# Kernel optimization log

Measured on AMD Instinct MI355X. Metric: run time of the kernel, lower is better.

Reference implementation:

```python
import jax, jax.numpy as jnp
import numpy as np

Q_HEADS = 16
KV_HEADS = 4
ROPE_THETA = 10000.0


def _rope(x, seq_len):
    # x: [B, S, H, D]; pairs are consecutive along D (view_as_complex semantics)
    D = x.shape[-1]
    inv_freq = 1.0 / (ROPE_THETA ** (jnp.arange(0, D, 2, dtype=jnp.float32) / D))
    freqs = jnp.arange(seq_len, dtype=jnp.float32)[:, None] * inv_freq  # [S, D/2]
    cos = jnp.cos(freqs)[None, :, None, :]
    sin = jnp.sin(freqs)[None, :, None, :]
    xr = x.reshape(x.shape[:-1] + (D // 2, 2))
    x0, x1 = xr[..., 0], xr[..., 1]
    out = jnp.stack([x0 * cos - x1 * sin, x0 * sin + x1 * cos], axis=-1)
    return out.reshape(x.shape)


def setup_inputs() -> dict:
    key = jax.random.key(0)
    ks = jax.random.split(key, 6)
    B, S, E = 1, 2048, 2048
    KV_DIM = KV_HEADS * (E // Q_HEADS)  # 512
    scale = 0.02
    return {
        "x": jax.random.normal(ks[0], (B, S, E), dtype=jnp.float32),
        "Wq": jax.random.normal(ks[1], (E, E), dtype=jnp.float32) * scale,
        "Wk": jax.random.normal(ks[2], (KV_DIM, E), dtype=jnp.float32) * scale,
        "Wv": jax.random.normal(ks[3], (KV_DIM, E), dtype=jnp.float32) * scale,
        "Wo": jax.random.normal(ks[4], (E, E), dtype=jnp.float32) * scale,
        "bo": jax.random.normal(ks[5], (E,), dtype=jnp.float32) * scale,
        "cache_keys": jnp.zeros((B, S, KV_HEADS, E // Q_HEADS), dtype=jnp.float32),
        "cache_value": jnp.zeros((B, S, KV_HEADS, E // Q_HEADS), dtype=jnp.float32),
        "start_pos": 0,
    }


def reference(x, Wq, Wk, Wv, Wo, bo, cache_keys, cache_value, start_pos):
    B, S, E = x.shape
    hd = E // Q_HEADS
    G = Q_HEADS // KV_HEADS  # queries per kv head

    xq = (x @ Wq.T).reshape(B, S, Q_HEADS, hd)
    xk = (x @ Wk.T).reshape(B, S, KV_HEADS, hd)
    xv = (x @ Wv.T).reshape(B, S, KV_HEADS, hd)

    # Original applies RoPE with positions 0..seq_len-1 for both q and k
    # (freq tensor is sliced [:seq_len] inside apply_rotry_position_embedding).
    xq = _rope(xq, S)
    xk = _rope(xk, S)

    # cache write at start_pos (static python int)
    cache_keys = jax.lax.dynamic_update_slice(cache_keys, xk, (0, start_pos, 0, 0))
    cache_value = jax.lax.dynamic_update_slice(cache_value, xv, (0, start_pos, 0, 0))
    total = start_pos + S
    k_full = cache_keys[:, :total]   # [B, T, KVH, hd]
    v_full = cache_value[:, :total]

    # repeat_interleave over the head axis == GQA expansion
    k = jnp.repeat(k_full, G, axis=2)  # [B, T, QH, hd]
    v = jnp.repeat(v_full, G, axis=2)

    scores = jnp.einsum("bshd,bthd->bhst", xq, k) / jnp.sqrt(jnp.float32(hd))
    causal = jnp.triu(jnp.ones((S, total), dtype=bool), k=1)  # [S, T]
    scores = jnp.where(causal[None, None, :, :], -jnp.inf, scores)
    weights = jax.nn.softmax(scores, axis=-1)
    out = jnp.einsum("bhst,bthd->bshd", weights, v).reshape(B, S, E)
    # dropout p=0.0 / eval mode -> identity
    return out @ Wo.T + bo
```

## Files before the change

### kernel.cpp

```cpp
#include <hip/hip_runtime.h>
#include <stdint.h>

typedef unsigned short u16;
typedef float  f32x4  __attribute__((ext_vector_type(4)));
typedef __bf16 bf16x8 __attribute__((ext_vector_type(8)));
typedef __bf16 bf16x4 __attribute__((ext_vector_type(4)));
typedef unsigned short u16x8 __attribute__((ext_vector_type(8)));
typedef unsigned short u16x4v __attribute__((ext_vector_type(4)));

#define S_LEN 2048
#define E_DIM 2048
#define HD    128
#define QH    16
#define KVH   4
#define KVD   512
#define NQKV  3072
#define QK_SCALE 0.08838834764831845f

#define AS1 __attribute__((address_space(1)))
#define AS3 __attribute__((address_space(3)))

__device__ __forceinline__ u16 f2bf(float f) {
  union { float f; uint32_t u; } v; v.f = f;
  return (u16)((v.u + 0x7FFFu + ((v.u >> 16) & 1u)) >> 16);
}

__global__ void cast_all_kernel(const float* __restrict__ x, const float* __restrict__ Wq,
                                const float* __restrict__ Wk, const float* __restrict__ Wv,
                                const float* __restrict__ Wo,
                                u16* __restrict__ xb, u16* __restrict__ Wcat,
                                u16* __restrict__ Wob, float2* __restrict__ tab) {
  int i = blockIdx.x * blockDim.x + threadIdx.x;
  if (i >= 3670016) {
    int j = i - 3670016;
    int s = j >> 6, pidx = j & 63;
    float inv = exp2f((float)pidx * (-13.287712379549449f / 64.0f));
    float sn, cs;
    sincosf((float)s * inv, &sn, &cs);
    tab[j] = make_float2(cs, sn);
    return;
  }
  const float* src; u16* dst;
  if (i < (1 << 20))                       { src = x  + (size_t)i * 4;  dst = xb + (size_t)i * 4; }
  else if (i < (2 << 20))                  { size_t j = i - (1 << 20);  src = Wq + j * 4; dst = Wcat + j * 4; }
  else if (i < (2 << 20) + (1 << 18))      { size_t j = i - (2 << 20);  src = Wk + j * 4; dst = Wcat + (size_t)E_DIM * E_DIM + j * 4; }
  else if (i < (2 << 20) + (2 << 18))      { size_t j = i - (2 << 20) - (1 << 18); src = Wv + j * 4; dst = Wcat + (size_t)(E_DIM + KVD) * E_DIM + j * 4; }
  else                                     { size_t j = i - (2 << 20) - (2 << 18); src = Wo + j * 4; dst = Wob + j * 4; }
  float4 f = *reinterpret_cast<const float4*>(src);
  u16x4v o;
  o[0] = f2bf(f.x); o[1] = f2bf(f.y); o[2] = f2bf(f.z); o[3] = f2bf(f.w);
  *reinterpret_cast<u16x4v*>(dst) = o;
}

template<bool BIAS, int MODE>
__global__ __launch_bounds__(256) void gemm_bt_kernel(
    const u16* __restrict__ A, const u16* __restrict__ B,
    float* __restrict__ C, const float* __restrict__ bias,
    const float2* __restrict__ tab, u16* __restrict__ qb,
    u16* __restrict__ kb, u16* __restrict__ vTp,
    int M, int N, int K)
{
  __shared__ u16 As[2][64 * 64];
  __shared__ u16 Bs[2][128 * 64];

  const int tid  = threadIdx.x;
  const int lane = tid & 63;
  const int wid  = tid >> 6;
  const int wc   = wid * 32;
  const int lr   = lane & 15;
  const int kg   = lane >> 4;
  const int sw   = lr & 7;

  const int bm = blockIdx.y * 64;
  const int bn = blockIdx.x * 128;

  f32x4 acc[4][2];
  #pragma unroll
  for (int r = 0; r < 4; ++r)
    #pragma unroll
    for (int c = 0; c < 2; ++c) acc[r][c] = (f32x4){0.f, 0.f, 0.f, 0.f};

  const int srow   = wid * 8 + (lane >> 3);
  const int schunk = (lane & 7) ^ (lane >> 3);

  const u16* gA = A + (size_t)(bm + srow) * K + schunk * 8;
  const u16* gB = B + (size_t)(bn + srow) * K + schunk * 8;

  auto stage = [&](int buf, int kt) {
    #pragma unroll
    for (int i = 0; i < 2; ++i)
      __builtin_amdgcn_global_load_lds(
          (const AS1 void*)(gA + (size_t)i * 32 * K + kt),
          (AS3 void*)(&As[buf][(wid*8 + i*32) * 64]), 16, 0, 0);
    #pragma unroll
    for (int i = 0; i < 4; ++i)
      __builtin_amdgcn_global_load_lds(
          (const AS1 void*)(gB + (size_t)i * 32 * K + kt),
          (AS3 void*)(&Bs[buf][(wid*8 + i*32) * 64]), 16, 0, 0);
  };

  stage(0, 0);
  __syncthreads();

  int cur = 0;
  for (int kt = 0; kt < K; kt += 64) {
    if (kt + 64 < K) stage(cur ^ 1, kt + 64);
    #pragma unroll
    for (int kk = 0; kk < 2; ++kk) {
      bf16x8 af[4], bfr[2];
      #pragma unroll
      for (int r = 0; r < 4; ++r)
        af[r] = *reinterpret_cast<const bf16x8*>(
            &As[cur][(r*16 + lr)*64 + ((kk*4 + kg) ^ sw)*8]);
      #pragma unroll
      for (int c = 0; c < 2; ++c)
        bfr[c] = *reinterpret_cast<const bf16x8*>(
            &Bs[cur][(wc + c*16 + lr)*64 + ((kk*4 + kg) ^ sw)*8]);
      #pragma unroll
      for (int r = 0; r < 4; ++r)
        #pragma unroll
        for (int c = 0; c < 2; ++c)
          acc[r][c] = __builtin_amdgcn_mfma_f32_16x16x32_bf16(af[r], bfr[c], acc[r][c], 0, 0, 0);
    }
    __syncthreads();
    cur ^= 1;
  }

  const int crow = kg * 4;
  #pragma unroll
  for (int r = 0; r < 4; ++r) {
    #pragma unroll
    for (int c = 0; c < 2; ++c) {
      int gr = bm + r*16 + crow;
      int gc = bn + wc + c*16 + lr;
      if constexpr (MODE == 0) {
        float badd = BIAS ? bias[gc] : 0.0f;
        #pragma unroll
        for (int reg = 0; reg < 4; ++reg)
          C[(size_t)(gr + reg)*N + gc] = acc[r][c][reg] + badd;
      } else {
        if (gc < E_DIM + KVD) {
          int pidx = (gc & 127) >> 1;
          bool odd = lr & 1;
          #pragma unroll
          for (int reg = 0; reg < 4; ++reg) {
            float val = acc[r][c][reg];
            float oth = __shfl_xor(val, 1);
            float2 cs = tab[(gr + reg) * 64 + pidx];
            float o = odd ? (oth * cs.y + val * cs.x)
                          : (val * cs.x - oth * cs.y);
            if (gc < E_DIM)
              qb[(size_t)(gr + reg) * E_DIM + gc] = f2bf(o * QK_SCALE);
            else
              kb[(size_t)(gr + reg) * KVD + (gc - E_DIM)] = f2bf(o);
          }
        } else {
          bf16x4 pk;
          #pragma unroll
          for (int reg = 0; reg < 4; ++reg) pk[reg] = (__bf16)acc[r][c][reg];
          *reinterpret_cast<bf16x4*>(
              &vTp[(size_t)(gc - E_DIM - KVD) * S_LEN + gr]) = pk;
        }
      }
    }
  }
}

__device__ __forceinline__ void attn_tile(
    int t, int qt, int wid, int lr, int kg,
    const bf16x8* qf, f32x4* o, float& mr, float& ls,
    const u16* ks, const u16* vts, u16* ps)
{
  const int sw = lr & 7;
  f32x4 st[4];
  #pragma unroll
  for (int c = 0; c < 4; ++c) st[c] = (f32x4){0.f, 0.f, 0.f, 0.f};
  __builtin_amdgcn_s_setprio(1);
  #pragma unroll
  for (int kk = 0; kk < 4; ++kk) {
    #pragma unroll
    for (int c = 0; c < 4; ++c) {
      bf16x8 kfr = *reinterpret_cast<const bf16x8*>(
          &ks[(c*16 + lr)*128 + ((kk*4 + kg) ^ sw)*8]);
      st[c] = __builtin_amdgcn_mfma_f32_16x16x32_bf16(kfr, qf[kk], st[c], 0, 0, 0);
    }
  }
  __builtin_amdgcn_s_setprio(0);
  if (t == qt) {
    #pragma unroll
    for (int c = 0; c < 4; ++c)
      #pragma unroll
      for (int reg = 0; reg < 4; ++reg)
        if (c*16 + kg*4 + reg > wid*16 + lr) st[c][reg] = -1e30f;
  }
  float cm[4];
  #pragma unroll
  for (int c = 0; c < 4; ++c)
    cm[c] = fmaxf(fmaxf(st[c][0], st[c][1]), fmaxf(st[c][2], st[c][3]));
  float pm = fmaxf(fmaxf(cm[0], cm[1]), fmaxf(cm[2], cm[3]));
  pm = fmaxf(pm, __shfl_xor(pm, 16));
  pm = fmaxf(pm, __shfl_xor(pm, 32));

  if (!__all(pm - mr <= 8.0f)) {
    float nm = fmaxf(mr, pm);
    float alpha = __expf(mr - nm);
    ls *= alpha;
    mr = nm;
    float ar[4];
    #pragma unroll
    for (int reg = 0; reg < 4; ++reg)
      ar[reg] = __shfl(alpha, kg*4 + reg);
    #pragma unroll
    for (int d = 0; d < 8; ++d)
      #pragma unroll
      for (int reg = 0; reg < 4; ++reg)
        o[d][reg] *= ar[reg];
  }

  float p[4][4];
  float csum[4];
  #pragma unroll
  for (int c = 0; c < 4; ++c) {
    #pragma unroll
    for (int reg = 0; reg < 4; ++reg)
      p[c][reg] = __expf(st[c][reg] - mr);
    csum[c] = (p[c][0] + p[c][1]) + (p[c][2] + p[c][3]);
  }
  float sum = (csum[0] + csum[1]) + (csum[2] + csum[3]);
  sum += __shfl_xor(sum, 16);
  sum += __shfl_xor(sum, 32);
  ls += sum;

  #pragma unroll
  for (int c = 0; c < 4; ++c) {
    bf16x4 pk;
    #pragma unroll
    for (int reg = 0; reg < 4; ++reg) pk[reg] = (__bf16)p[c][reg];
    *reinterpret_cast<bf16x4*>(&ps[lr*72 + c*16 + kg*4]) = pk;
  }
  __builtin_amdgcn_s_setprio(1);
  #pragma unroll
  for (int kk = 0; kk < 2; ++kk) {
    bf16x8 pa = *reinterpret_cast<const bf16x8*>(&ps[lr*72 + kk*32 + kg*8]);
    #pragma unroll
    for (int d = 0; d < 8; ++d) {
      bf16x8 vb = *reinterpret_cast<const bf16x8*>(
          &vts[(d*16 + lr)*64 + ((kk*4 + kg) ^ sw)*8]);
      o[d] = __builtin_amdgcn_mfma_f32_16x16x32_bf16(pa, vb, o[d], 0, 0, 0);
    }
  }
  __builtin_amdgcn_s_setprio(0);
}

__global__ __launch_bounds__(256, 2) void attn_kernel(
    const u16* __restrict__ Q, const u16* __restrict__ Kc,
    const u16* __restrict__ VT, u16* __restrict__ Out)
{
  __shared__ u16 Ks[2][64 * 128];
  __shared__ u16 VTs[2][128 * 64];
  __shared__ u16 Ps[4][16 * 72];

  const int x = blockIdx.x;
  int qt, h;
  if (x < 256) { qt = x & 31; h = x >> 5; }
  else         { int xp = x - 256; qt = 31 - (xp & 31); h = 8 + (xp >> 5); }
  const int kvh = h >> 2;
  const int tid  = threadIdx.x;
  const int lane = tid & 63;
  const int wid  = tid >> 6;
  const int lr   = lane & 15;
  const int kg   = lane >> 4;

  const int NT = qt + 1;

  bf16x8 qf[4];
  {
    const u16* qa = Q + (size_t)(qt*64 + wid*16 + lr) * E_DIM + h * HD + kg * 8;
    #pragma unroll
    for (int kk = 0; kk < 4; ++kk)
      qf[kk] = *reinterpret_cast<const bf16x8*>(qa + kk * 32);
  }

  f32x4 o[8];
  #pragma unroll
  for (int d = 0; d < 8; ++d) o[d] = (f32x4){0.f,0.f,0.f,0.f};
  float mr = -1e30f, ls = 0.f;

  u16x8 kreg[4], vreg[4];
  const u16* kbase = Kc + kvh * HD;
  const u16* vbase = VT + (size_t)(kvh * HD) * S_LEN;

  auto stage_load = [&](int t) {
    #pragma unroll
    for (int i = 0; i < 4; ++i) {
      int c = i * 256 + tid;
      kreg[i] = *reinterpret_cast<const u16x8*>(
          kbase + (size_t)(t*64 + (c >> 4)) * KVD + (c & 15) * 8);
      vreg[i] = *reinterpret_cast<const u16x8*>(
          vbase + (size_t)(c >> 3) * S_LEN + t*64 + (c & 7) * 8);
    }
  };
  auto stage_write = [&](int b) {
    #pragma unroll
    for (int i = 0; i < 4; ++i) {
      int c = i * 256 + tid;
      int kr = c >> 4, kc = c & 15;
      *reinterpret_cast<u16x8*>(&Ks[b][kr*128 + (kc ^ (kr & 7))*8]) = kreg[i];
      int vr = c >> 3, vc = c & 7;
      *reinterpret_cast<u16x8*>(&VTs[b][vr*64 + (vc ^ (vr & 7))*8]) = vreg[i];
    }
  };

  int p = 0;
  stage_load(0);
  stage_write(0);
  __syncthreads();

  for (int t = 0; t < NT; ++t) {
    if (t + 1 < NT) stage_load(t + 1);
    attn_tile(t, qt, wid, lr, kg, qf, o, mr, ls, Ks[p], VTs[p], Ps[wid]);
    if (t + 1 < NT) {
      stage_write(p ^ 1);
      __syncthreads();
      p ^= 1;
    }
  }

  {
    float inv = 1.0f / ls;
    float ivq[4];
    #pragma unroll
    for (int reg = 0; reg < 4; ++reg)
      ivq[reg] = __shfl(inv, kg*4 + reg);
    #pragma unroll
    for (int reg = 0; reg < 4; ++reg) {
      int grow = qt*64 + wid*16 + kg*4 + reg;
      #pragma unroll
      for (int d = 0; d < 8; ++d)
        Out[(size_t)grow * E_DIM + h * HD + d*16 + lr] =
            __builtin_bit_cast(u16, (__bf16)(o[d][reg] * ivq[reg]));
    }
  }
}

extern "C" void kernel_launch(void* const* d_in, const int* in_sizes, int n_in,
                              void* d_out, int out_size, void* d_ws, size_t ws_size,
                              hipStream_t stream)
{
  const float* x  = (const float*)d_in[0];
  const float* Wq = (const float*)d_in[1];
  const float* Wk = (const float*)d_in[2];
  const float* Wv = (const float*)d_in[3];
  const float* Wo = (const float*)d_in[4];
  const float* bo = (const float*)d_in[5];
  float* out = (float*)d_out;

  char* w = (char*)d_ws;
  u16*    xb   = (u16*)(w);
  u16*    Wcat = (u16*)(w + (8u  << 20));
  u16*    Wob  = (u16*)(w + (20u << 20));
  float2* tab  = (float2*)(w + (28u << 20));
  u16*    qb   = (u16*)(w + (30u << 20));
  u16*    kb   = (u16*)(w + (38u << 20));
  u16*    vT   = (u16*)(w + (40u << 20));
  u16*    attn = (u16*)(w + (42u << 20));
  (void)ws_size; (void)in_sizes; (void)n_in; (void)out_size;

  cast_all_kernel<<<14848, 256, 0, stream>>>(x, Wq, Wk, Wv, Wo, xb, Wcat, Wob, tab);

  gemm_bt_kernel<false, 2><<<dim3(NQKV/128, S_LEN/64), 256, 0, stream>>>(
      xb, Wcat, nullptr, nullptr, tab, qb, kb, vT, S_LEN, NQKV, E_DIM);

  attn_kernel<<<512, 256, 0, stream>>>(qb, kb, vT, attn);

  gemm_bt_kernel<true, 0><<<dim3(E_DIM/128, S_LEN/64), 256, 0, stream>>>(
      attn, Wob, out, bo, nullptr, nullptr, nullptr, nullptr, S_LEN, E_DIM, E_DIM);
}
```

Before: 133.8 us.

## Switch attention to 32x32x16 MFMA with split-KV waves and final merge

Rewrites the attention inner loop to use 32x32x16 bf16 MFMA instead of 16x16x32. The four waves now form a 2x2 grid: two 32-row query groups times two 32-column halves of each KV tile. Each wave keeps its own online-softmax state, and the halves are merged through shared memory at the end. The P tile is rearranged into the A-operand layout with cross-lane shuffles rather than an LDS round trip, which removes the Ps buffer. This is meant to cut LDS traffic and MFMA instruction count per tile, at the cost of more accumulator registers, an extra epilogue sync and merge, and per-wave softmax state.

```diff
diff --git a/kernel.cpp b/kernel.cpp
--- a/kernel.cpp
+++ b/kernel.cpp
@@ -3,10 +3,13 @@
 
 typedef unsigned short u16;
 typedef float  f32x4  __attribute__((ext_vector_type(4)));
+typedef float  f32x16 __attribute__((ext_vector_type(16)));
 typedef __bf16 bf16x8 __attribute__((ext_vector_type(8)));
 typedef __bf16 bf16x4 __attribute__((ext_vector_type(4)));
 typedef unsigned short u16x8 __attribute__((ext_vector_type(8)));
 typedef unsigned short u16x4v __attribute__((ext_vector_type(4)));
+typedef unsigned int u32x2 __attribute__((ext_vector_type(2)));
+typedef unsigned int u32x4 __attribute__((ext_vector_type(4)));
 
 #define S_LEN 2048
 #define E_DIM 2048
@@ -166,99 +169,12 @@
   }
 }
 
-__device__ __forceinline__ void attn_tile(
-    int t, int qt, int wid, int lr, int kg,
-    const bf16x8* qf, f32x4* o, float& mr, float& ls,
-    const u16* ks, const u16* vts, u16* ps)
-{
-  const int sw = lr & 7;
-  f32x4 st[4];
-  #pragma unroll
-  for (int c = 0; c < 4; ++c) st[c] = (f32x4){0.f, 0.f, 0.f, 0.f};
-  __builtin_amdgcn_s_setprio(1);
-  #pragma unroll
-  for (int kk = 0; kk < 4; ++kk) {
-    #pragma unroll
-    for (int c = 0; c < 4; ++c) {
-      bf16x8 kfr = *reinterpret_cast<const bf16x8*>(
-          &ks[(c*16 + lr)*128 + ((kk*4 + kg) ^ sw)*8]);
-      st[c] = __builtin_amdgcn_mfma_f32_16x16x32_bf16(kfr, qf[kk], st[c], 0, 0, 0);
-    }
-  }
-  __builtin_amdgcn_s_setprio(0);
-  if (t == qt) {
-    #pragma unroll
-    for (int c = 0; c < 4; ++c)
-      #pragma unroll
-      for (int reg = 0; reg < 4; ++reg)
-        if (c*16 + kg*4 + reg > wid*16 + lr) st[c][reg] = -1e30f;
-  }
-  float cm[4];
-  #pragma unroll
-  for (int c = 0; c < 4; ++c)
-    cm[c] = fmaxf(fmaxf(st[c][0], st[c][1]), fmaxf(st[c][2], st[c][3]));
-  float pm = fmaxf(fmaxf(cm[0], cm[1]), fmaxf(cm[2], cm[3]));
-  pm = fmaxf(pm, __shfl_xor(pm, 16));
-  pm = fmaxf(pm, __shfl_xor(pm, 32));
-
-  if (!__all(pm - mr <= 8.0f)) {
-    float nm = fmaxf(mr, pm);
-    float alpha = __expf(mr - nm);
-    ls *= alpha;
-    mr = nm;
-    float ar[4];
-    #pragma unroll
-    for (int reg = 0; reg < 4; ++reg)
-      ar[reg] = __shfl(alpha, kg*4 + reg);
-    #pragma unroll
-    for (int d = 0; d < 8; ++d)
-      #pragma unroll
-      for (int reg = 0; reg < 4; ++reg)
-        o[d][reg] *= ar[reg];
-  }
-
-  float p[4][4];
-  float csum[4];
-  #pragma unroll
-  for (int c = 0; c < 4; ++c) {
-    #pragma unroll
-    for (int reg = 0; reg < 4; ++reg)
-      p[c][reg] = __expf(st[c][reg] - mr);
-    csum[c] = (p[c][0] + p[c][1]) + (p[c][2] + p[c][3]);
-  }
-  float sum = (csum[0] + csum[1]) + (csum[2] + csum[3]);
-  sum += __shfl_xor(sum, 16);
-  sum += __shfl_xor(sum, 32);
-  ls += sum;
-
-  #pragma unroll
-  for (int c = 0; c < 4; ++c) {
-    bf16x4 pk;
-    #pragma unroll
-    for (int reg = 0; reg < 4; ++reg) pk[reg] = (__bf16)p[c][reg];
-    *reinterpret_cast<bf16x4*>(&ps[lr*72 + c*16 + kg*4]) = pk;
-  }
-  __builtin_amdgcn_s_setprio(1);
-  #pragma unroll
-  for (int kk = 0; kk < 2; ++kk) {
-    bf16x8 pa = *reinterpret_cast<const bf16x8*>(&ps[lr*72 + kk*32 + kg*8]);
-    #pragma unroll
-    for (int d = 0; d < 8; ++d) {
-      bf16x8 vb = *reinterpret_cast<const bf16x8*>(
-          &vts[(d*16 + lr)*64 + ((kk*4 + kg) ^ sw)*8]);
-      o[d] = __builtin_amdgcn_mfma_f32_16x16x32_bf16(pa, vb, o[d], 0, 0, 0);
-    }
-  }
-  __builtin_amdgcn_s_setprio(0);
-}
-
 __global__ __launch_bounds__(256, 2) void attn_kernel(
     const u16* __restrict__ Q, const u16* __restrict__ Kc,
     const u16* __restrict__ VT, u16* __restrict__ Out)
 {
   __shared__ u16 Ks[2][64 * 128];
   __shared__ u16 VTs[2][128 * 64];
-  __shared__ u16 Ps[4][16 * 72];
 
   const int x = blockIdx.x;
   int qt, h;
@@ -268,22 +184,26 @@
   const int tid  = threadIdx.x;
   const int lane = tid & 63;
   const int wid  = tid >> 6;
-  const int lr   = lane & 15;
-  const int kg   = lane >> 4;
+  const int kvg  = wid & 1;
+  const int rowg = wid >> 1;
+  const int ln   = lane & 31;
+  const int hi   = lane >> 5;
 
   const int NT = qt + 1;
 
-  bf16x8 qf[4];
+  bf16x8 qf[8];
   {
-    const u16* qa = Q + (size_t)(qt*64 + wid*16 + lr) * E_DIM + h * HD + kg * 8;
-    #pragma unroll
-    for (int kk = 0; kk < 4; ++kk)
-      qf[kk] = *reinterpret_cast<const bf16x8*>(qa + kk * 32);
-  }
-
-  f32x4 o[8];
+    const u16* qa = Q + (size_t)(qt*64 + rowg*32 + ln) * E_DIM + h * HD + hi * 8;
+    #pragma unroll
+    for (int ks = 0; ks < 8; ++ks)
+      qf[ks] = *reinterpret_cast<const bf16x8*>(qa + ks * 16);
+  }
+
+  f32x16 o4[4];
   #pragma unroll
-  for (int d = 0; d < 8; ++d) o[d] = (f32x4){0.f,0.f,0.f,0.f};
+  for (int d = 0; d < 4; ++d)
+    #pragma unroll
+    for (int r = 0; r < 16; ++r) o4[d][r] = 0.f;
   float mr = -1e30f, ls = 0.f;
 
   u16x8 kreg[4], vreg[4];
@@ -316,9 +236,96 @@
   stage_write(0);
   __syncthreads();
 
+  const int krow = kvg*32 + ln;
+
   for (int t = 0; t < NT; ++t) {
     if (t + 1 < NT) stage_load(t + 1);
-    attn_tile(t, qt, wid, lr, kg, qf, o, mr, ls, Ks[p], VTs[p], Ps[wid]);
+
+    f32x16 st;
+    #pragma unroll
+    for (int r = 0; r < 16; ++r) st[r] = 0.f;
+    __builtin_amdgcn_s_setprio(1);
+    #pragma unroll
+    for (int ks = 0; ks < 8; ++ks) {
+      bf16x8 kfr = *reinterpret_cast<const bf16x8*>(
+          &Ks[p][krow*128 + ((ks*2 + hi) ^ (ln & 7))*8]);
+      st = __builtin_amdgcn_mfma_f32_32x32x16_bf16(kfr, qf[ks], st, 0, 0, 0);
+    }
+    __builtin_amdgcn_s_setprio(0);
+
+    if (t == qt) {
+      #pragma unroll
+      for (int reg = 0; reg < 16; ++reg) {
+        int kvl = kvg*32 + 4*hi + (reg & 3) + 8*(reg >> 2);
+        if (kvl > rowg*32 + ln) st[reg] = -1e30f;
+      }
+    }
+
+    float pm = -1e30f;
+    #pragma unroll
+    for (int reg = 0; reg < 16; ++reg) pm = fmaxf(pm, st[reg]);
+    pm = fmaxf(pm, __shfl_xor(pm, 32));
+
+    if (!__all(pm - mr <= 8.0f)) {
+      float nm = fmaxf(mr, pm);
+      float alpha = __expf(mr - nm);
+      ls *= alpha;
+      mr = nm;
+      #pragma unroll
+      for (int reg = 0; reg < 16; ++reg) {
+        int crow = (reg & 3) + 8*(reg >> 2) + 4*hi;
+        float ar = __shfl(alpha, crow);
+        #pragma unroll
+        for (int d = 0; d < 4; ++d) o4[d][reg] *= ar;
+      }
+    }
+
+    float pv[16];
+    float sum = 0.f;
+    #pragma unroll
+    for (int reg = 0; reg < 16; ++reg) {
+      pv[reg] = __expf(st[reg] - mr);
+      sum += pv[reg];
+    }
+    sum += __shfl_xor(sum, 32);
+    ls += sum;
+
+    bf16x8 pa[2];
+    #pragma unroll
+    for (int ks = 0; ks < 2; ++ks) {
+      bf16x4 A4, B4;
+      #pragma unroll
+      for (int j = 0; j < 4; ++j) {
+        A4[j] = (__bf16)pv[ks*8 + j];
+        B4[j] = (__bf16)pv[ks*8 + 4 + j];
+      }
+      u32x2 uA = __builtin_bit_cast(u32x2, A4);
+      u32x2 uB = __builtin_bit_cast(u32x2, B4);
+      unsigned sx = hi ? uA[0] : uB[0];
+      unsigned sy = hi ? uA[1] : uB[1];
+      unsigned rx = __shfl_xor(sx, 32);
+      unsigned ry = __shfl_xor(sy, 32);
+      u32x4 w;
+      w[0] = hi ? rx : uA[0];
+      w[1] = hi ? ry : uA[1];
+      w[2] = hi ? uB[0] : rx;
+      w[3] = hi ? uB[1] : ry;
+      pa[ks] = __builtin_bit_cast(bf16x8, w);
+    }
+
+    __builtin_amdgcn_s_setprio(1);
+    #pragma unroll
+    for (int d = 0; d < 4; ++d) {
+      int vrow = d*32 + ln;
+      #pragma unroll
+      for (int ks = 0; ks < 2; ++ks) {
+        bf16x8 vb = *reinterpret_cast<const bf16x8*>(
+            &VTs[p][vrow*64 + ((kvg*4 + ks*2 + hi) ^ (ln & 7))*8]);
+        o4[d] = __builtin_amdgcn_mfma_f32_32x32x16_bf16(pa[ks], vb, o4[d], 0, 0, 0);
+      }
+    }
+    __builtin_amdgcn_s_setprio(0);
+
     if (t + 1 < NT) {
       stage_write(p ^ 1);
       __syncthreads();
@@ -326,19 +333,41 @@
     }
   }
 
-  {
-    float inv = 1.0f / ls;
-    float ivq[4];
-    #pragma unroll
-    for (int reg = 0; reg < 4; ++reg)
-      ivq[reg] = __shfl(inv, kg*4 + reg);
-    #pragma unroll
-    for (int reg = 0; reg < 4; ++reg) {
-      int grow = qt*64 + wid*16 + kg*4 + reg;
-      #pragma unroll
-      for (int d = 0; d < 8; ++d)
-        Out[(size_t)grow * E_DIM + h * HD + d*16 + lr] =
-            __builtin_bit_cast(u16, (__bf16)(o[d][reg] * ivq[reg]));
+  __syncthreads();
+  float* Obuf = (float*)&Ks[0][0];
+  float* Lbuf = (float*)&VTs[0][0];
+  if (kvg == 1) {
+    if (hi == 0) { Lbuf[rowg*32 + ln] = mr; Lbuf[64 + rowg*32 + ln] = ls; }
+    #pragma unroll
+    for (int reg = 0; reg < 16; ++reg) {
+      int crow = (reg & 3) + 8*(reg >> 2) + 4*hi;
+      #pragma unroll
+      for (int d = 0; d < 4; ++d)
+        Obuf[(rowg*32 + crow)*128 + d*32 + ln] = o4[d][reg];
+    }
+  }
+  __syncthreads();
+  if (kvg == 0) {
+    float mB = Lbuf[rowg*32 + ln];
+    float lB = Lbuf[64 + rowg*32 + ln];
+    float m  = fmaxf(mr, mB);
+    float a0 = __expf(mr - m);
+    float a1 = __expf(mB - m);
+    float inv = 1.0f / (ls*a0 + lB*a1);
+    #pragma unroll
+    for (int reg = 0; reg < 16; ++reg) {
+      int crow = (reg & 3) + 8*(reg >> 2) + 4*hi;
+      float a0r = __shfl(a0, crow);
+      float a1r = __shfl(a1, crow);
+      float ivr = __shfl(inv, crow);
+      int grow = qt*64 + rowg*32 + crow;
+      #pragma unroll
+      for (int d = 0; d < 4; ++d) {
+        float v = (o4[d][reg]*a0r +
+                   Obuf[(rowg*32 + crow)*128 + d*32 + ln]*a1r) * ivr;
+        Out[(size_t)grow * E_DIM + h * HD + d*32 + ln] =
+            __builtin_bit_cast(u16, (__bf16)v);
+      }
     }
   }
 }
```

New measurement: 130.1 us. 2.8% less time.
